# Performance work log

Hardware: AMD Instinct MI355X
Metric: run time of the kernel (lower is better)

The kernel has to match this reference:

```python
import jax, jax.numpy as jnp
import numpy as np


def _conv1x1_prelu(x, w, b, a):
    # 1x1 conv == channel matmul; PReLU with shared scalar slope a
    y = jnp.einsum('oc,nchw->nohw', w, x) + b[None, :, None, None]
    return jnp.where(y >= 0, y, a * y)


def setup_inputs() -> dict:
    key = jax.random.key(0)
    ks = jax.random.split(key, 7)
    N, C, H, W = 2, 128, 96, 96
    Ce = 64  # channel // reduction
    s_in = 1.0 / np.sqrt(C)
    return {
        'input': jax.random.normal(ks[0], (N, C, H, W), jnp.float32),
        'w1': jax.random.normal(ks[1], (Ce, C), jnp.float32) * s_in,
        'b1': jnp.zeros((Ce,), jnp.float32),
        'a1': jnp.full((1,), 0.25, jnp.float32),
        'w2': jax.random.normal(ks[2], (Ce, C), jnp.float32) * s_in,
        'b2': jnp.zeros((Ce,), jnp.float32),
        'a2': jnp.full((1,), 0.25, jnp.float32),
        'wa': jax.random.normal(ks[3], (C, C), jnp.float32) * s_in,
        'ba': jnp.zeros((C,), jnp.float32),
        'aa': jnp.full((1,), 0.25, jnp.float32),
    }


def reference(input, w1, b1, a1, w2, b2, a2, wa, ba, aa):
    e1 = _conv1x1_prelu(input, w1, b1, a1[0])  # [N, Ce, H, W]
    e2 = _conv1x1_prelu(input, w2, b2, a2[0])  # [N, Ce, H, W]
    xa = _conv1x1_prelu(input, wa, ba, aa[0])  # [N, C,  H, W]
    N, Ce, H, W = e1.shape
    HW = H * W
    q = e1.transpose(0, 2, 3, 1).reshape(N, HW, Ce)   # [N, HW, Ce]
    k = e2.reshape(N, Ce, HW)                          # [N, Ce, HW]
    score = jax.nn.softmax(jnp.matmul(q, k), axis=-1)  # [N, HW, HW] (no scale, as in source)
    v = xa.reshape(N, -1, HW).transpose(0, 2, 1)       # [N, HW, C]
    out = jnp.matmul(score, v)                         # [N, HW, C]
    return out.transpose(0, 2, 1).reshape(N, -1, H, W)
```

## Files before the change

### kernel.cpp

```cpp
#include <hip/hip_runtime.h>
#include <cstdint>
#include <cstddef>

#define HW_ 9216
#define CC 128
#define NQT 144
#define NQT2 72
#define LOG2E 1.44269504088896f

typedef short bf16x8 __attribute__((ext_vector_type(8)));
typedef unsigned short u16x4 __attribute__((ext_vector_type(4)));
typedef unsigned short u16x8 __attribute__((ext_vector_type(8)));
typedef float f32x4 __attribute__((ext_vector_type(4)));

__device__ __forceinline__ unsigned short f2bf(float f) {
    unsigned int u = __builtin_bit_cast(unsigned int, f);
    u += 0x7FFFu + ((u >> 16) & 1u);
    return (unsigned short)(u >> 16);
}

__device__ __forceinline__ float fast_exp2(float x) {
#if __has_builtin(__builtin_amdgcn_exp2f)
    return __builtin_amdgcn_exp2f(x);
#else
    return exp2f(x);
#endif
}

__device__ __forceinline__ unsigned int cvt_pk_bf16(float lo, float hi) {
    unsigned int r;
    asm("v_cvt_pk_bf16_f32 %0, %1, %2" : "=v"(r) : "v"(lo), "v"(hi));
    return r;
}

__global__ __launch_bounds__(256) void prep_w(const float* __restrict__ w1,
                                              const float* __restrict__ w2,
                                              const float* __restrict__ wa,
                                              float* __restrict__ wt) {
    int idx = blockIdx.x * 256 + threadIdx.x;
    int o = idx >> 7, c = idx & 127;
    float v;
    if (o < 64)       v = w1[o * 128 + c];
    else if (o < 128) v = w2[(o - 64) * 128 + c];
    else              v = wa[(o - 128) * 128 + c];
    wt[c * 256 + o] = v;
}

__global__ __launch_bounds__(256) void conv_kernel(
    const float* __restrict__ x, const float* __restrict__ wt,
    const float* __restrict__ b1, const float* __restrict__ a1,
    const float* __restrict__ b2, const float* __restrict__ a2,
    const float* __restrict__ ba, const float* __restrict__ aa,
    unsigned short* __restrict__ qb, unsigned short* __restrict__ kb,
    unsigned short* __restrict__ vtb) {
    const int ptile = blockIdx.x;
    const int oset  = blockIdx.y;
    const int n     = blockIdx.z;
    const int t = threadIdx.x;
    const int p = t & 63;
    const int og = __builtin_amdgcn_readfirstlane(t >> 6);
    const int p0 = ptile * 64;

    __shared__ float xs[128 * 64];
    {
        const int cs = t >> 4, p4 = (t & 15) * 4;
#pragma unroll
        for (int c = cs; c < 128; c += 16) {
            float4 v = *(const float4*)(x + ((size_t)n * CC + c) * HW_ + p0 + p4);
            *(float4*)&xs[c * 64 + p4] = v;
        }
    }
    __syncthreads();

    const int obase = oset * 64 + og * 16;
    float acc[16];
#pragma unroll
    for (int i = 0; i < 16; i++) acc[i] = 0.f;

#pragma unroll 8
    for (int c = 0; c < 128; c++) {
        float xv = xs[c * 64 + p];
        const float* wr = wt + c * 256 + obase;
#pragma unroll
        for (int i = 0; i < 16; i++) acc[i] = fmaf(wr[i], xv, acc[i]);
    }

    const float* bias_p;
    const float* slope_p;
    if (oset == 0)      { bias_p = b1; slope_p = a1; }
    else if (oset == 1) { bias_p = b2; slope_p = a2; }
    else                { bias_p = ba; slope_p = aa; }
    const float slope = slope_p[0];

    unsigned short vals[16];
#pragma unroll
    for (int i = 0; i < 16; i++) {
        float bv = (oset < 2) ? bias_p[og * 16 + i] : bias_p[obase - 128 + i];
        float y = acc[i] + bv;
        y = (y >= 0.f) ? y : slope * y;
        if (oset == 0) y *= LOG2E;
        vals[i] = f2bf(y);
    }

    if (oset < 2) {
        unsigned short* dst = (oset == 0 ? qb : kb) + ((size_t)n * HW_ + p0 + p) * 64 + og * 16;
        bf16x8 v0, v1;
#pragma unroll
        for (int i = 0; i < 8; i++) { v0[i] = (short)vals[i]; v1[i] = (short)vals[8 + i]; }
        *(bf16x8*)(dst)     = v0;
        *(bf16x8*)(dst + 8) = v1;
    } else {
        int c0 = obase - 128;
#pragma unroll
        for (int i = 0; i < 16; i++)
            vtb[((size_t)n * CC + c0 + i) * HW_ + p0 + p] = vals[i];
    }
}

__global__ __launch_bounds__(256, 2) void attn_kernel(
    const unsigned short* __restrict__ qb, const unsigned short* __restrict__ kb,
    const unsigned short* __restrict__ vtb,
    float* __restrict__ o_part, float* __restrict__ l_part,
    int nch, int chunk_j) {
    const int qt    = blockIdx.x;
    const int chunk = blockIdx.y;
    const int n     = blockIdx.z;
    const int t = threadIdx.x;
    const int w = t >> 6;
    const int lane = t & 63;
    const int l15 = lane & 15;
    const int quad = lane >> 4;
    const int e7 = l15 & 7;

    __shared__ __align__(16) unsigned short k_lds[64 * 64];
    __shared__ __align__(16) unsigned short v_lds[128 * 64];
    __shared__ __align__(16) unsigned short p_lds[4 * 1024];

    const int row_ga = qt * 128 + w * 32 + l15;
    const int row_gb = row_ga + 16;
    const bf16x8 bq0a = *(const bf16x8*)(qb + ((size_t)n * HW_ + row_ga) * 64 + quad * 8);
    const bf16x8 bq1a = *(const bf16x8*)(qb + ((size_t)n * HW_ + row_ga) * 64 + 32 + quad * 8);
    const bf16x8 bq0b = *(const bf16x8*)(qb + ((size_t)n * HW_ + row_gb) * 64 + quad * 8);
    const bf16x8 bq1b = *(const bf16x8*)(qb + ((size_t)n * HW_ + row_gb) * 64 + 32 + quad * 8);

    f32x4 acc_oa[8], acc_ob[8];
#pragma unroll
    for (int i = 0; i < 8; i++) {
        acc_oa[i] = (f32x4){0.f, 0.f, 0.f, 0.f};
        acc_ob[i] = (f32x4){0.f, 0.f, 0.f, 0.f};
    }
    float l_sa = 0.f, l_sb = 0.f;

    const int stg_row = t >> 3, stg_seg = t & 7;
    const int iters = chunk_j / 64;
    int j0 = chunk * chunk_j;

    bf16x8 kr0, kr1, vr0, vr1, vr2, vr3;
    {
        const unsigned short* kp = kb + ((size_t)n * HW_ + j0 + stg_row) * 64 + stg_seg * 8;
        kr0 = *(const bf16x8*)kp;
        kr1 = *(const bf16x8*)(kp + 32 * 64);
        const unsigned short* vp = vtb + ((size_t)n * CC + stg_row) * HW_ + j0 + stg_seg * 8;
        vr0 = *(const bf16x8*)vp;
        vr1 = *(const bf16x8*)(vp + (size_t)32 * HW_);
        vr2 = *(const bf16x8*)(vp + (size_t)64 * HW_);
        vr3 = *(const bf16x8*)(vp + (size_t)96 * HW_);
    }

    for (int it = 0; it < iters; ++it, j0 += 64) {
        __syncthreads();
        {
            int r0 = stg_row, r1 = stg_row + 32;
            *(bf16x8*)&k_lds[r0 * 64 + ((stg_seg ^ (r0 & 7)) * 8)] = kr0;
            *(bf16x8*)&k_lds[r1 * 64 + ((stg_seg ^ (r1 & 7)) * 8)] = kr1;
            *(bf16x8*)&v_lds[r0 * 64 + ((stg_seg ^ (r0 & 7)) * 8)] = vr0;
            *(bf16x8*)&v_lds[r1 * 64 + ((stg_seg ^ (r1 & 7)) * 8)] = vr1;
            int r2 = stg_row + 64, r3 = stg_row + 96;
            *(bf16x8*)&v_lds[r2 * 64 + ((stg_seg ^ (r2 & 7)) * 8)] = vr2;
            *(bf16x8*)&v_lds[r3 * 64 + ((stg_seg ^ (r3 & 7)) * 8)] = vr3;
        }
        __syncthreads();

        if (it + 1 < iters) {
            const unsigned short* kp = kb + ((size_t)n * HW_ + j0 + 64 + stg_row) * 64 + stg_seg * 8;
            kr0 = *(const bf16x8*)kp;
            kr1 = *(const bf16x8*)(kp + 32 * 64);
            const unsigned short* vp = vtb + ((size_t)n * CC + stg_row) * HW_ + j0 + 64 + stg_seg * 8;
            vr0 = *(const bf16x8*)vp;
            vr1 = *(const bf16x8*)(vp + (size_t)32 * HW_);
            vr2 = *(const bf16x8*)(vp + (size_t)64 * HW_);
            vr3 = *(const bf16x8*)(vp + (size_t)96 * HW_);
        }

        f32x4 sa[4], sb[4];
#pragma unroll
        for (int ct = 0; ct < 4; ct++) {
            int jr = ct * 16 + l15;
            bf16x8 ak0 = *(const bf16x8*)&k_lds[jr * 64 + ((quad ^ e7) * 8)];
            bf16x8 ak1 = *(const bf16x8*)&k_lds[jr * 64 + (((4 + quad) ^ e7) * 8)];
            f32x4 za = (f32x4){0.f, 0.f, 0.f, 0.f};
            za = __builtin_amdgcn_mfma_f32_16x16x32_bf16(ak0, bq0a, za, 0, 0, 0);
            za = __builtin_amdgcn_mfma_f32_16x16x32_bf16(ak1, bq1a, za, 0, 0, 0);
            sa[ct] = za;
            f32x4 zb = (f32x4){0.f, 0.f, 0.f, 0.f};
            zb = __builtin_amdgcn_mfma_f32_16x16x32_bf16(ak0, bq0b, zb, 0, 0, 0);
            zb = __builtin_amdgcn_mfma_f32_16x16x32_bf16(ak1, bq1b, zb, 0, 0, 0);
            sb[ct] = zb;
        }

#pragma unroll
        for (int ct = 0; ct < 4; ct++) {
            sa[ct][0] = fast_exp2(sa[ct][0]);
            sa[ct][1] = fast_exp2(sa[ct][1]);
            sa[ct][2] = fast_exp2(sa[ct][2]);
            sa[ct][3] = fast_exp2(sa[ct][3]);
        }
        {
            float u0 = sa[0][0] + sa[0][1], u1 = sa[0][2] + sa[0][3];
            float u2 = sa[1][0] + sa[1][1], u3 = sa[1][2] + sa[1][3];
            float u4 = sa[2][0] + sa[2][1], u5 = sa[2][2] + sa[2][3];
            float u6 = sa[3][0] + sa[3][1], u7 = sa[3][2] + sa[3][3];
            float v0 = u0 + u1, v1 = u2 + u3, v2 = u4 + u5, v3 = u6 + u7;
            l_sa += (v0 + v1) + (v2 + v3);
        }
#pragma unroll
        for (int ct = 0; ct < 4; ct++) {
            unsigned int pk01 = cvt_pk_bf16(sa[ct][0], sa[ct][1]);
            unsigned int pk23 = cvt_pk_bf16(sa[ct][2], sa[ct][3]);
            int chunkid = 2 * ct + (quad >> 1);
            int off = l15 * 64 + ((chunkid ^ e7) * 8) + 4 * (quad & 1);
            uint2 tmp;
            tmp.x = pk01;
            tmp.y = pk23;
            *(u16x4*)&p_lds[w * 1024 + off] = __builtin_bit_cast(u16x4, tmp);
        }
        asm volatile("" ::: "memory");
        const bf16x8 bp0a = __builtin_bit_cast(bf16x8,
            *(const u16x8*)&p_lds[w * 1024 + l15 * 64 + ((quad ^ e7) * 8)]);
        const bf16x8 bp1a = __builtin_bit_cast(bf16x8,
            *(const u16x8*)&p_lds[w * 1024 + l15 * 64 + (((4 + quad) ^ e7) * 8)]);
        asm volatile("" ::: "memory");

#pragma unroll
        for (int ct = 0; ct < 4; ct++) {
            sb[ct][0] = fast_exp2(sb[ct][0]);
            sb[ct][1] = fast_exp2(sb[ct][1]);
            sb[ct][2] = fast_exp2(sb[ct][2]);
            sb[ct][3] = fast_exp2(sb[ct][3]);
        }
        {
            float u0 = sb[0][0] + sb[0][1], u1 = sb[0][2] + sb[0][3];
            float u2 = sb[1][0] + sb[1][1], u3 = sb[1][2] + sb[1][3];
            float u4 = sb[2][0] + sb[2][1], u5 = sb[2][2] + sb[2][3];
            float u6 = sb[3][0] + sb[3][1], u7 = sb[3][2] + sb[3][3];
            float v0 = u0 + u1, v1 = u2 + u3, v2 = u4 + u5, v3 = u6 + u7;
            l_sb += (v0 + v1) + (v2 + v3);
        }
#pragma unroll
        for (int ct = 0; ct < 4; ct++) {
            unsigned int pk01 = cvt_pk_bf16(sb[ct][0], sb[ct][1]);
            unsigned int pk23 = cvt_pk_bf16(sb[ct][2], sb[ct][3]);
            int chunkid = 2 * ct + (quad >> 1);
            int off = l15 * 64 + ((chunkid ^ e7) * 8) + 4 * (quad & 1);
            uint2 tmp;
            tmp.x = pk01;
            tmp.y = pk23;
            *(u16x4*)&p_lds[w * 1024 + off] = __builtin_bit_cast(u16x4, tmp);
        }
        asm volatile("" ::: "memory");
        const bf16x8 bp0b = __builtin_bit_cast(bf16x8,
            *(const u16x8*)&p_lds[w * 1024 + l15 * 64 + ((quad ^ e7) * 8)]);
        const bf16x8 bp1b = __builtin_bit_cast(bf16x8,
            *(const u16x8*)&p_lds[w * 1024 + l15 * 64 + (((4 + quad) ^ e7) * 8)]);
        asm volatile("" ::: "memory");

        __builtin_amdgcn_s_setprio(1);
#pragma unroll
        for (int ctv = 0; ctv < 8; ctv++) {
            int cr = ctv * 16 + l15;
            bf16x8 av0 = *(const bf16x8*)&v_lds[cr * 64 + ((quad ^ e7) * 8)];
            bf16x8 av1 = *(const bf16x8*)&v_lds[cr * 64 + (((4 + quad) ^ e7) * 8)];
            acc_oa[ctv] = __builtin_amdgcn_mfma_f32_16x16x32_bf16(av0, bp0a, acc_oa[ctv], 0, 0, 0);
            acc_oa[ctv] = __builtin_amdgcn_mfma_f32_16x16x32_bf16(av1, bp1a, acc_oa[ctv], 0, 0, 0);
            acc_ob[ctv] = __builtin_amdgcn_mfma_f32_16x16x32_bf16(av0, bp0b, acc_ob[ctv], 0, 0, 0);
            acc_ob[ctv] = __builtin_amdgcn_mfma_f32_16x16x32_bf16(av1, bp1b, acc_ob[ctv], 0, 0, 0);
        }
        __builtin_amdgcn_s_setprio(0);
    }

    l_sa += __shfl_xor(l_sa, 16);
    l_sa += __shfl_xor(l_sa, 32);
    l_sb += __shfl_xor(l_sb, 16);
    l_sb += __shfl_xor(l_sb, 32);

    const size_t cbase = ((size_t)(n * NQT2 + qt) * nch + chunk) * 128;
    const int qla = w * 32 + l15, qlb = qla + 16;
#pragma unroll
    for (int ctv = 0; ctv < 8; ctv++)
#pragma unroll
        for (int r = 0; r < 4; r++) {
            int c = ctv * 16 + 4 * quad + r;
            o_part[(cbase + c) * 128 + qla] = acc_oa[ctv][r];
            o_part[(cbase + c) * 128 + qlb] = acc_ob[ctv][r];
        }
    if (quad == 0) {
        size_t lb = ((size_t)(n * NQT2 + qt) * nch + chunk) * 128;
        l_part[lb + qla] = l_sa;
        l_part[lb + qlb] = l_sb;
    }
}

__global__ __launch_bounds__(256) void combine_kernel(
    const float* __restrict__ o_part, const float* __restrict__ lp,
    float* __restrict__ out, int nch) {
    int gid = blockIdx.x * 256 + threadIdx.x;
    int r4 = (gid & 31) * 4;
    int rest = gid >> 5;
    int c = rest & 127;
    int nqt = rest >> 7;
    int n = nqt / NQT2, qtp = nqt - n * NQT2;

    float4 num = {0.f, 0.f, 0.f, 0.f}, den = {0.f, 0.f, 0.f, 0.f};
    for (int ch = 0; ch < nch; ch++) {
        float4 o = *(const float4*)&o_part[(((size_t)nqt * nch + ch) * 128 + c) * 128 + r4];
        float4 l = *(const float4*)&lp[((size_t)nqt * nch + ch) * 128 + r4];
        num.x += o.x; num.y += o.y; num.z += o.z; num.w += o.w;
        den.x += l.x; den.y += l.y; den.z += l.z; den.w += l.w;
    }
    float4 res;
    res.x = num.x / den.x;
    res.y = num.y / den.y;
    res.z = num.z / den.z;
    res.w = num.w / den.w;
    *(float4*)&out[((size_t)n * CC + c) * HW_ + qtp * 128 + r4] = res;
}

extern "C" void kernel_launch(void* const* d_in, const int* in_sizes, int n_in,
                              void* d_out, int out_size, void* d_ws, size_t ws_size,
                              hipStream_t stream) {
    const float* x  = (const float*)d_in[0];
    const float* w1 = (const float*)d_in[1];
    const float* b1 = (const float*)d_in[2];
    const float* a1 = (const float*)d_in[3];
    const float* w2 = (const float*)d_in[4];
    const float* b2 = (const float*)d_in[5];
    const float* a2 = (const float*)d_in[6];
    const float* wa = (const float*)d_in[7];
    const float* ba = (const float*)d_in[8];
    const float* aa = (const float*)d_in[9];
    float* out = (float*)d_out;

    auto need = [](int nc) -> size_t {
        return 9568256ull + (size_t)nc * 9437184ull + (size_t)nc * 73728ull;
    };
    int nch;
    if (ws_size >= need(6))      nch = 6;
    else if (ws_size >= need(4)) nch = 4;
    else                         nch = 2;
    const int chunk_j = HW_ / nch;

    char* ws = (char*)d_ws;
    float*          wt     = (float*)(ws + 0);
    unsigned short* qb     = (unsigned short*)(ws + 131072);
    unsigned short* kb     = (unsigned short*)(ws + 2490368);
    unsigned short* vtb    = (unsigned short*)(ws + 4849664);
    float*          o_part = (float*)(ws + 9568256);
    float*          lpart  = (float*)(ws + 9568256 + (size_t)nch * 9437184);

    hipLaunchKernelGGL(prep_w, dim3(128), dim3(256), 0, stream, w1, w2, wa, wt);
    hipLaunchKernelGGL(conv_kernel, dim3(144, 4, 2), dim3(256), 0, stream,
                       x, wt, b1, a1, b2, a2, ba, aa, qb, kb, vtb);
    hipLaunchKernelGGL(attn_kernel, dim3(NQT2, nch, 2), dim3(256), 0, stream,
                       qb, kb, vtb, o_part, lpart, nch, chunk_j);
    hipLaunchKernelGGL(combine_kernel, dim3(2 * NQT2 * 128 * 128 / (256 * 4)), dim3(256), 0, stream,
                       o_part, lpart, out, nch);
}
```

Measured before the change: 190.1 us.

## Compute 1x1 convs with split-bf16 MFMA and LDS-staged coalesced stores

The scalar FP32 FMA conv kernel is replaced by bf16 MFMA, using a hi/lo split of both weights and inputs (three MFMAs per tile) to keep roughly FP32 accuracy. Each block now computes all 256 output channels for a 64-pixel tile, so the grid shrinks from 4 output sets to 1 and input x is read once per tile. Results are staged in LDS so q, k and the transposed v are written with coalesced 16-byte stores. The cost is extra MFMA work, a hi/lo conversion step and higher LDS use, which limits occupancy to one block per CU.

New measurement: 183.4 us. 1.04x faster.

```diff
diff --git a/kernel.cpp b/kernel.cpp
--- a/kernel.cpp
+++ b/kernel.cpp
@@ -17,6 +17,10 @@
     unsigned int u = __builtin_bit_cast(unsigned int, f);
     u += 0x7FFFu + ((u >> 16) & 1u);
     return (unsigned short)(u >> 16);
+}
+
+__device__ __forceinline__ float bf2f(unsigned short h) {
+    return __builtin_bit_cast(float, (unsigned int)h << 16);
 }
 
 __device__ __forceinline__ float fast_exp2(float x) {
@@ -36,84 +40,128 @@
 __global__ __launch_bounds__(256) void prep_w(const float* __restrict__ w1,
                                               const float* __restrict__ w2,
                                               const float* __restrict__ wa,
-                                              float* __restrict__ wt) {
+                                              unsigned short* __restrict__ wh,
+                                              unsigned short* __restrict__ wl) {
     int idx = blockIdx.x * 256 + threadIdx.x;
     int o = idx >> 7, c = idx & 127;
     float v;
     if (o < 64)       v = w1[o * 128 + c];
     else if (o < 128) v = w2[(o - 64) * 128 + c];
     else              v = wa[(o - 128) * 128 + c];
-    wt[c * 256 + o] = v;
-}
-
-__global__ __launch_bounds__(256) void conv_kernel(
-    const float* __restrict__ x, const float* __restrict__ wt,
+    unsigned short h = f2bf(v);
+    unsigned short l = f2bf(v - bf2f(h));
+    wh[o * 128 + c] = h;
+    wl[o * 128 + c] = l;
+}
+
+__global__ __launch_bounds__(256, 1) void conv_kernel(
+    const float* __restrict__ x,
+    const unsigned short* __restrict__ wh, const unsigned short* __restrict__ wl,
     const float* __restrict__ b1, const float* __restrict__ a1,
     const float* __restrict__ b2, const float* __restrict__ a2,
     const float* __restrict__ ba, const float* __restrict__ aa,
     unsigned short* __restrict__ qb, unsigned short* __restrict__ kb,
     unsigned short* __restrict__ vtb) {
     const int ptile = blockIdx.x;
-    const int oset  = blockIdx.y;
-    const int n     = blockIdx.z;
+    const int n     = blockIdx.y;
     const int t = threadIdx.x;
-    const int p = t & 63;
-    const int og = __builtin_amdgcn_readfirstlane(t >> 6);
+    const int w = t >> 6;
+    const int lane = t & 63;
+    const int l15 = lane & 15;
+    const int quad = lane >> 4;
     const int p0 = ptile * 64;
 
-    __shared__ float xs[128 * 64];
+    __shared__ __align__(16) unsigned short xh[64 * 136];
+    __shared__ __align__(16) unsigned short xl[64 * 136];
+    __shared__ __align__(16) unsigned short os[4 * 64 * 72];
+
     {
-        const int cs = t >> 4, p4 = (t & 15) * 4;
-#pragma unroll
-        for (int c = cs; c < 128; c += 16) {
-            float4 v = *(const float4*)(x + ((size_t)n * CC + c) * HW_ + p0 + p4);
-            *(float4*)&xs[c * 64 + p4] = v;
+        const int cs = t >> 4;
+        const int p4 = (t & 15) * 4;
+#pragma unroll
+        for (int cc = cs; cc < 128; cc += 16) {
+            float4 v = *(const float4*)(x + ((size_t)n * CC + cc) * HW_ + p0 + p4);
+            float vv[4] = {v.x, v.y, v.z, v.w};
+#pragma unroll
+            for (int j = 0; j < 4; j++) {
+                unsigned short h = f2bf(vv[j]);
+                unsigned short l = f2bf(vv[j] - bf2f(h));
+                xh[(p4 + j) * 136 + cc] = h;
+                xl[(p4 + j) * 136 + cc] = l;
+            }
         }
     }
     __syncthreads();
 
-    const int obase = oset * 64 + og * 16;
-    float acc[16];
-#pragma unroll
-    for (int i = 0; i < 16; i++) acc[i] = 0.f;
-
-#pragma unroll 8
-    for (int c = 0; c < 128; c++) {
-        float xv = xs[c * 64 + p];
-        const float* wr = wt + c * 256 + obase;
-#pragma unroll
-        for (int i = 0; i < 16; i++) acc[i] = fmaf(wr[i], xv, acc[i]);
-    }
-
-    const float* bias_p;
-    const float* slope_p;
-    if (oset == 0)      { bias_p = b1; slope_p = a1; }
-    else if (oset == 1) { bias_p = b2; slope_p = a2; }
-    else                { bias_p = ba; slope_p = aa; }
+    f32x4 acc[4][4];
+#pragma unroll
+    for (int ot = 0; ot < 4; ot++)
+#pragma unroll
+        for (int pt = 0; pt < 4; pt++) acc[ot][pt] = (f32x4){0.f, 0.f, 0.f, 0.f};
+
+#pragma unroll
+    for (int k = 0; k < 4; k++) {
+        bf16x8 bh[4], bl[4];
+#pragma unroll
+        for (int ot = 0; ot < 4; ot++) {
+            const size_t woff = (size_t)(w * 64 + ot * 16 + l15) * 128 + k * 32 + quad * 8;
+            bh[ot] = *(const bf16x8*)(wh + woff);
+            bl[ot] = *(const bf16x8*)(wl + woff);
+        }
+#pragma unroll
+        for (int pt = 0; pt < 4; pt++) {
+            const int aoff = (pt * 16 + l15) * 136 + k * 32 + quad * 8;
+            bf16x8 ah = *(const bf16x8*)&xh[aoff];
+            bf16x8 al = *(const bf16x8*)&xl[aoff];
+#pragma unroll
+            for (int ot = 0; ot < 4; ot++) {
+                acc[ot][pt] = __builtin_amdgcn_mfma_f32_16x16x32_bf16(ah, bh[ot], acc[ot][pt], 0, 0, 0);
+                acc[ot][pt] = __builtin_amdgcn_mfma_f32_16x16x32_bf16(ah, bl[ot], acc[ot][pt], 0, 0, 0);
+                acc[ot][pt] = __builtin_amdgcn_mfma_f32_16x16x32_bf16(al, bh[ot], acc[ot][pt], 0, 0, 0);
+            }
+        }
+    }
+
+    const float* bias_p  = (w == 0) ? b1 : (w == 1) ? b2 : ba;
+    const float* slope_p = (w == 0) ? a1 : (w == 1) ? a2 : aa;
     const float slope = slope_p[0];
-
-    unsigned short vals[16];
-#pragma unroll
-    for (int i = 0; i < 16; i++) {
-        float bv = (oset < 2) ? bias_p[og * 16 + i] : bias_p[obase - 128 + i];
-        float y = acc[i] + bv;
-        y = (y >= 0.f) ? y : slope * y;
-        if (oset == 0) y *= LOG2E;
-        vals[i] = f2bf(y);
-    }
-
-    if (oset < 2) {
-        unsigned short* dst = (oset == 0 ? qb : kb) + ((size_t)n * HW_ + p0 + p) * 64 + og * 16;
-        bf16x8 v0, v1;
-#pragma unroll
-        for (int i = 0; i < 8; i++) { v0[i] = (short)vals[i]; v1[i] = (short)vals[8 + i]; }
-        *(bf16x8*)(dst)     = v0;
-        *(bf16x8*)(dst + 8) = v1;
-    } else {
-        int c0 = obase - 128;
-#pragma unroll
-        for (int i = 0; i < 16; i++)
-            vtb[((size_t)n * CC + c0 + i) * HW_ + p0 + p] = vals[i];
+    unsigned short* osw = os + w * 64 * 72;
+
+#pragma unroll
+    for (int ot = 0; ot < 4; ot++) {
+        const int bidx = (w < 2 ? 0 : (w - 2) * 64) + ot * 16 + l15;
+        const float bv = bias_p[bidx];
+#pragma unroll
+        for (int pt = 0; pt < 4; pt++) {
+            unsigned short us[4];
+#pragma unroll
+            for (int r = 0; r < 4; r++) {
+                float y = acc[ot][pt][r] + bv;
+                y = (y >= 0.f) ? y : slope * y;
+                if (w == 0) y *= LOG2E;
+                us[r] = f2bf(y);
+            }
+            if (w < 2) {
+#pragma unroll
+                for (int r = 0; r < 4; r++)
+                    osw[(pt * 16 + quad * 4 + r) * 72 + ot * 16 + l15] = us[r];
+            } else {
+                u16x4 pk = {us[0], us[1], us[2], us[3]};
+                *(u16x4*)&osw[(ot * 16 + l15) * 72 + pt * 16 + quad * 4] = pk;
+            }
+        }
+    }
+    asm volatile("" ::: "memory");
+
+    const unsigned short* src = osw + lane * 72;
+    unsigned short* dst;
+    if (w == 0)      dst = qb + ((size_t)n * HW_ + p0 + lane) * 64;
+    else if (w == 1) dst = kb + ((size_t)n * HW_ + p0 + lane) * 64;
+    else             dst = vtb + ((size_t)(n * CC + (w - 2) * 64 + lane)) * HW_ + p0;
+#pragma unroll
+    for (int j = 0; j < 8; j++) {
+        u16x8 v = *(const u16x8*)(src + j * 8);
+        *(u16x8*)(dst + j * 8) = v;
     }
 }
 
@@ -360,16 +408,17 @@
     const int chunk_j = HW_ / nch;
 
     char* ws = (char*)d_ws;
-    float*          wt     = (float*)(ws + 0);
+    unsigned short* wh     = (unsigned short*)(ws + 0);
+    unsigned short* wl     = (unsigned short*)(ws + 65536);
     unsigned short* qb     = (unsigned short*)(ws + 131072);
     unsigned short* kb     = (unsigned short*)(ws + 2490368);
     unsigned short* vtb    = (unsigned short*)(ws + 4849664);
     float*          o_part = (float*)(ws + 9568256);
     float*          lpart  = (float*)(ws + 9568256 + (size_t)nch * 9437184);
 
-    hipLaunchKernelGGL(prep_w, dim3(128), dim3(256), 0, stream, w1, w2, wa, wt);
-    hipLaunchKernelGGL(conv_kernel, dim3(144, 4, 2), dim3(256), 0, stream,
-                       x, wt, b1, a1, b2, a2, ba, aa, qb, kb, vtb);
+    hipLaunchKernelGGL(prep_w, dim3(128), dim3(256), 0, stream, w1, w2, wa, wh, wl);
+    hipLaunchKernelGGL(conv_kernel, dim3(144, 2), dim3(256), 0, stream,
+                       x, wh, wl, b1, a1, b2, a2, ba, aa, qb, kb, vtb);
     hipLaunchKernelGGL(attn_kernel, dim3(NQT2, nch, 2), dim3(256), 0, stream,
                        qb, kb, vtb, o_part, lpart, nch, chunk_j);
     hipLaunchKernelGGL(combine_kernel, dim3(2 * NQT2 * 128 * 128 / (256 * 4)), dim3(256), 0, stream,
```
